# Kernel tuning notes

Measured on AMD Instinct MI355X. Metric: run time of the kernel, lower is better.

## Reference

```python
import jax, jax.numpy as jnp
import numpy as np

HALF_LOG_2PI = 0.5 * float(np.log(2.0 * np.pi))


def setup_inputs() -> dict:
    key = jax.random.key(0)
    k1, k2 = jax.random.split(key)
    N, D = 16384, 2048
    x = jax.random.normal(k1, (N, D), dtype=jnp.float32)
    raw_params = jax.random.normal(k2, (2 * D,), dtype=jnp.float32)
    # chain spanning tree: edges (i, i+1) for i in 0..D-2  -> shape [D-1, 2]
    idx = jnp.arange(D - 1, dtype=jnp.int64)
    edges = jnp.stack([idx, idx + 1], axis=1)
    return {"x": x, "raw_params": raw_params, "edges": edges}


def reference(x, raw_params, edges):
    # x: [N, D] float; raw_params: [2D] float; edges: [E, 2] int
    D = x.shape[1]
    means = jnp.tanh(raw_params[:D]) * 2.0               # [D]
    stds = jax.nn.softplus(raw_params[D:]) + 1e-6         # [D]
    # Each edge (i, j) contributes logN(x_i) + logN(x_j); equivalently each
    # feature k contributes deg(k) * logN(x_k), deg = endpoint multiplicity.
    deg = jnp.zeros((D,), dtype=x.dtype).at[edges.reshape(-1)].add(1.0)  # [D]
    z = (x - means) / stds                                # [N, D]
    logp = -0.5 * z * z - jnp.log(stds) - HALF_LOG_2PI    # [N, D]
    return logp @ deg                                     # [N]
```

## Files before the change

kernel.cpp:

```cpp
#include <hip/hip_runtime.h>
#include <math.h>

#define HALF_LOG_2PI_F 0.9189385332046727f

typedef float f32x4 __attribute__((ext_vector_type(4)));

template <int NI>
__global__ __launch_bounds__(256) void clt_fused(
        const float* __restrict__ x,
        const float* __restrict__ rp,
        const int* __restrict__ edges,
        float* __restrict__ out,
        int D, int E, int N, int total_waves) {
    extern __shared__ __align__(16) float smem[];
    float* sdeg = smem;
    float* As   = smem + D;
    float* Bs   = smem + 2 * D;

    const int tid = threadIdx.x;

    for (int k = tid; k < D; k += 256) sdeg[k] = 0.0f;
    __syncthreads();
    for (int e = tid; e < E; e += 256) {
        atomicAdd(&sdeg[edges[2 * e]], 1.0f);
        atomicAdd(&sdeg[edges[2 * e + 1]], 1.0f);
    }
    __syncthreads();

    float local_c = 0.0f;
    for (int k = tid; k < D; k += 256) {
        float m = tanhf(rp[k]) * 2.0f;
        float sx = rp[D + k];
        float s = fmaxf(sx, 0.0f) + log1pf(expf(-fabsf(sx))) + 1e-6f;
        float inv_s2 = 1.0f / (s * s);
        float deg = sdeg[k];
        As[k] = deg * (-0.5f * inv_s2);
        Bs[k] = deg * (m * inv_s2);
        local_c += deg * (-0.5f * m * m * inv_s2 - logf(s) - HALF_LOG_2PI_F);
    }
#pragma unroll
    for (int off = 32; off > 0; off >>= 1)
        local_c += __shfl_down(local_c, off, 64);
    __shared__ float wsum[4];
    if ((tid & 63) == 0) wsum[tid >> 6] = local_c;
    __syncthreads();
    const float c = wsum[0] + wsum[1] + wsum[2] + wsum[3];

    const int lane = tid & 63;
    const f32x4* Av = (const f32x4*)As;
    const f32x4* Bv = (const f32x4*)Bs;
    f32x4 a4[NI], b4[NI];
#pragma unroll
    for (int i = 0; i < NI; ++i) {
        a4[i] = Av[i * 64 + lane];
        b4[i] = Bv[i * 64 + lane];
    }

    const int gwave = blockIdx.x * 4 + (tid >> 6);
    for (int r = gwave * 2; r < N; r += total_waves * 2) {
        const f32x4* xv0 = (const f32x4*)(x + (size_t)r * (size_t)D);
        const f32x4* xv1 = (const f32x4*)(x + (size_t)(r + 1) * (size_t)D);
        float p0 = 0.0f, q0 = 0.0f, p1 = 0.0f, q1 = 0.0f;
#pragma unroll
        for (int i = 0; i < NI; ++i) {
            f32x4 x0 = __builtin_nontemporal_load(&xv0[i * 64 + lane]);
            f32x4 x1 = __builtin_nontemporal_load(&xv1[i * 64 + lane]);
            p0 += x0.x * fmaf(a4[i].x, x0.x, b4[i].x);
            q0 += x0.y * fmaf(a4[i].y, x0.y, b4[i].y);
            p0 += x0.z * fmaf(a4[i].z, x0.z, b4[i].z);
            q0 += x0.w * fmaf(a4[i].w, x0.w, b4[i].w);
            p1 += x1.x * fmaf(a4[i].x, x1.x, b4[i].x);
            q1 += x1.y * fmaf(a4[i].y, x1.y, b4[i].y);
            p1 += x1.z * fmaf(a4[i].z, x1.z, b4[i].z);
            q1 += x1.w * fmaf(a4[i].w, x1.w, b4[i].w);
        }
        float acc0 = p0 + q0;
        float acc1 = p1 + q1;
#pragma unroll
        for (int off = 32; off > 0; off >>= 1) {
            acc0 += __shfl_down(acc0, off, 64);
            acc1 += __shfl_down(acc1, off, 64);
        }
        if (lane == 0) {
            out[r] = acc0 + c;
            out[r + 1] = acc1 + c;
        }
    }
}

__global__ void clt_prep_kernel(const float* __restrict__ rp,
                                const int* __restrict__ edges,
                                float* __restrict__ A,
                                float* __restrict__ B,
                                float* __restrict__ csum,
                                int D, int E) {
    extern __shared__ float sdeg[];
    for (int k = threadIdx.x; k < D; k += blockDim.x) sdeg[k] = 0.0f;
    __syncthreads();
    for (int e = threadIdx.x; e < E; e += blockDim.x) {
        atomicAdd(&sdeg[edges[2 * e]], 1.0f);
        atomicAdd(&sdeg[edges[2 * e + 1]], 1.0f);
    }
    __syncthreads();
    float local_c = 0.0f;
    for (int k = threadIdx.x; k < D; k += blockDim.x) {
        float m = tanhf(rp[k]) * 2.0f;
        float sx = rp[D + k];
        float s = fmaxf(sx, 0.0f) + log1pf(expf(-fabsf(sx))) + 1e-6f;
        float inv_s2 = 1.0f / (s * s);
        float deg = sdeg[k];
        A[k] = deg * (-0.5f * inv_s2);
        B[k] = deg * (m * inv_s2);
        local_c += deg * (-0.5f * m * m * inv_s2 - logf(s) - HALF_LOG_2PI_F);
    }
    __shared__ float wsum[16];
    for (int off = 32; off > 0; off >>= 1)
        local_c += __shfl_down(local_c, off, 64);
    if ((threadIdx.x & 63) == 0) wsum[threadIdx.x >> 6] = local_c;
    __syncthreads();
    if (threadIdx.x == 0) {
        float t = 0.0f;
        int nw = (blockDim.x + 63) >> 6;
        for (int w = 0; w < nw; ++w) t += wsum[w];
        *csum = t;
    }
}

__global__ __launch_bounds__(256) void clt_row_generic(
        const float* __restrict__ x,
        const float* __restrict__ A,
        const float* __restrict__ B,
        const float* __restrict__ csum,
        float* __restrict__ out,
        int D) {
    const int row = blockIdx.x;
    float acc = 0.0f;
    for (int k = threadIdx.x; k < D; k += blockDim.x) {
        float xs = x[(size_t)row * (size_t)D + k];
        acc += xs * fmaf(A[k], xs, B[k]);
    }
    for (int off = 32; off > 0; off >>= 1)
        acc += __shfl_down(acc, off, 64);
    __shared__ float wsum[4];
    if ((threadIdx.x & 63) == 0) wsum[threadIdx.x >> 6] = acc;
    __syncthreads();
    if (threadIdx.x == 0)
        out[row] = wsum[0] + wsum[1] + wsum[2] + wsum[3] + *csum;
}

extern "C" void kernel_launch(void* const* d_in, const int* in_sizes, int n_in,
                              void* d_out, int out_size, void* d_ws, size_t ws_size,
                              hipStream_t stream) {
    const float* x     = (const float*)d_in[0];
    const float* rp    = (const float*)d_in[1];
    const int*   edges = (const int*)d_in[2];
    float* out = (float*)d_out;

    const int D = in_sizes[1] / 2;
    const int E = in_sizes[2] / 2;
    const int N = out_size;

    const int NI = D / 256;
    const bool fast = (D % 256 == 0) && (N % 2 == 0) &&
                      (NI == 2 || NI == 4 || NI == 8 || NI == 16);
    if (fast) {
        const int blocks = 512;
        const int total_waves = blocks * 4;
        const size_t lds = (size_t)3 * D * sizeof(float);
        switch (NI) {
            case 2:  clt_fused<2><<<blocks, 256, lds, stream>>>(x, rp, edges, out, D, E, N, total_waves); break;
            case 4:  clt_fused<4><<<blocks, 256, lds, stream>>>(x, rp, edges, out, D, E, N, total_waves); break;
            case 8:  clt_fused<8><<<blocks, 256, lds, stream>>>(x, rp, edges, out, D, E, N, total_waves); break;
            default: clt_fused<16><<<blocks, 256, lds, stream>>>(x, rp, edges, out, D, E, N, total_waves); break;
        }
    } else {
        float* A    = (float*)d_ws;
        float* B    = A + D;
        float* csum = B + D;
        clt_prep_kernel<<<1, 1024, D * sizeof(float), stream>>>(rp, edges, A, B, csum, D, E);
        clt_row_generic<<<N, 256, 0, stream>>>(x, A, B, csum, out, D);
    }
}
```

Measured before the change: 39.44 us.

## Split parameter prep into separate kernel and drop per-block redundant prep

Replaces the fused kernel, in which every block recomputed the degree histogram and the A/B coefficients, with one single-block prep kernel that writes A, B and the constant to workspace. A streaming row kernel then reads those coefficients from global memory. The change also doubles the grid to 1024 blocks with a min-blocks launch bound, and switches the x loads from nontemporal to ordinary loads. It removes the per-block prep work and the LDS use, at the cost of an extra kernel launch and a serial dependency on one small single-block kernel.

Result: slower. 75.00 us (+90.1%).

```diff
diff --git a/kernel.cpp b/kernel.cpp
--- a/kernel.cpp
+++ b/kernel.cpp
@@ -4,89 +4,6 @@
 #define HALF_LOG_2PI_F 0.9189385332046727f
 
 typedef float f32x4 __attribute__((ext_vector_type(4)));
-
-template <int NI>
-__global__ __launch_bounds__(256) void clt_fused(
-        const float* __restrict__ x,
-        const float* __restrict__ rp,
-        const int* __restrict__ edges,
-        float* __restrict__ out,
-        int D, int E, int N, int total_waves) {
-    extern __shared__ __align__(16) float smem[];
-    float* sdeg = smem;
-    float* As   = smem + D;
-    float* Bs   = smem + 2 * D;
-
-    const int tid = threadIdx.x;
-
-    for (int k = tid; k < D; k += 256) sdeg[k] = 0.0f;
-    __syncthreads();
-    for (int e = tid; e < E; e += 256) {
-        atomicAdd(&sdeg[edges[2 * e]], 1.0f);
-        atomicAdd(&sdeg[edges[2 * e + 1]], 1.0f);
-    }
-    __syncthreads();
-
-    float local_c = 0.0f;
-    for (int k = tid; k < D; k += 256) {
-        float m = tanhf(rp[k]) * 2.0f;
-        float sx = rp[D + k];
-        float s = fmaxf(sx, 0.0f) + log1pf(expf(-fabsf(sx))) + 1e-6f;
-        float inv_s2 = 1.0f / (s * s);
-        float deg = sdeg[k];
-        As[k] = deg * (-0.5f * inv_s2);
-        Bs[k] = deg * (m * inv_s2);
-        local_c += deg * (-0.5f * m * m * inv_s2 - logf(s) - HALF_LOG_2PI_F);
-    }
-#pragma unroll
-    for (int off = 32; off > 0; off >>= 1)
-        local_c += __shfl_down(local_c, off, 64);
-    __shared__ float wsum[4];
-    if ((tid & 63) == 0) wsum[tid >> 6] = local_c;
-    __syncthreads();
-    const float c = wsum[0] + wsum[1] + wsum[2] + wsum[3];
-
-    const int lane = tid & 63;
-    const f32x4* Av = (const f32x4*)As;
-    const f32x4* Bv = (const f32x4*)Bs;
-    f32x4 a4[NI], b4[NI];
-#pragma unroll
-    for (int i = 0; i < NI; ++i) {
-        a4[i] = Av[i * 64 + lane];
-        b4[i] = Bv[i * 64 + lane];
-    }
-
-    const int gwave = blockIdx.x * 4 + (tid >> 6);
-    for (int r = gwave * 2; r < N; r += total_waves * 2) {
-        const f32x4* xv0 = (const f32x4*)(x + (size_t)r * (size_t)D);
-        const f32x4* xv1 = (const f32x4*)(x + (size_t)(r + 1) * (size_t)D);
-        float p0 = 0.0f, q0 = 0.0f, p1 = 0.0f, q1 = 0.0f;
-#pragma unroll
-        for (int i = 0; i < NI; ++i) {
-            f32x4 x0 = __builtin_nontemporal_load(&xv0[i * 64 + lane]);
-            f32x4 x1 = __builtin_nontemporal_load(&xv1[i * 64 + lane]);
-            p0 += x0.x * fmaf(a4[i].x, x0.x, b4[i].x);
-            q0 += x0.y * fmaf(a4[i].y, x0.y, b4[i].y);
-            p0 += x0.z * fmaf(a4[i].z, x0.z, b4[i].z);
-            q0 += x0.w * fmaf(a4[i].w, x0.w, b4[i].w);
-            p1 += x1.x * fmaf(a4[i].x, x1.x, b4[i].x);
-            q1 += x1.y * fmaf(a4[i].y, x1.y, b4[i].y);
-            p1 += x1.z * fmaf(a4[i].z, x1.z, b4[i].z);
-            q1 += x1.w * fmaf(a4[i].w, x1.w, b4[i].w);
-        }
-        float acc0 = p0 + q0;
-        float acc1 = p1 + q1;
-#pragma unroll
-        for (int off = 32; off > 0; off >>= 1) {
-            acc0 += __shfl_down(acc0, off, 64);
-            acc1 += __shfl_down(acc1, off, 64);
-        }
-        if (lane == 0) {
-            out[r] = acc0 + c;
-            out[r + 1] = acc1 + c;
-        }
-    }
-}
 
 __global__ void clt_prep_kernel(const float* __restrict__ rp,
                                 const int* __restrict__ edges,
@@ -126,6 +43,58 @@
     }
 }
 
+template <int NI>
+__global__ __launch_bounds__(256, 4) void clt_rows2(
+        const float* __restrict__ x,
+        const float* __restrict__ A,
+        const float* __restrict__ B,
+        const float* __restrict__ csum,
+        float* __restrict__ out,
+        int D, int N, int total_waves) {
+    const int lane = threadIdx.x & 63;
+    const int gwave = blockIdx.x * 4 + (threadIdx.x >> 6);
+
+    const f32x4* Av = (const f32x4*)A;
+    const f32x4* Bv = (const f32x4*)B;
+    f32x4 a4[NI], b4[NI];
+#pragma unroll
+    for (int i = 0; i < NI; ++i) {
+        a4[i] = Av[i * 64 + lane];
+        b4[i] = Bv[i * 64 + lane];
+    }
+    const float c = *csum;
+
+    for (int r = gwave * 2; r < N; r += total_waves * 2) {
+        const f32x4* xv0 = (const f32x4*)(x + (size_t)r * (size_t)D);
+        const f32x4* xv1 = (const f32x4*)(x + (size_t)(r + 1) * (size_t)D);
+        float p0 = 0.0f, q0 = 0.0f, p1 = 0.0f, q1 = 0.0f;
+#pragma unroll
+        for (int i = 0; i < NI; ++i) {
+            f32x4 x0 = xv0[i * 64 + lane];
+            f32x4 x1 = xv1[i * 64 + lane];
+            p0 += x0.x * fmaf(a4[i].x, x0.x, b4[i].x);
+            q0 += x0.y * fmaf(a4[i].y, x0.y, b4[i].y);
+            p0 += x0.z * fmaf(a4[i].z, x0.z, b4[i].z);
+            q0 += x0.w * fmaf(a4[i].w, x0.w, b4[i].w);
+            p1 += x1.x * fmaf(a4[i].x, x1.x, b4[i].x);
+            q1 += x1.y * fmaf(a4[i].y, x1.y, b4[i].y);
+            p1 += x1.z * fmaf(a4[i].z, x1.z, b4[i].z);
+            q1 += x1.w * fmaf(a4[i].w, x1.w, b4[i].w);
+        }
+        float acc0 = p0 + q0;
+        float acc1 = p1 + q1;
+#pragma unroll
+        for (int off = 32; off > 0; off >>= 1) {
+            acc0 += __shfl_down(acc0, off, 64);
+            acc1 += __shfl_down(acc1, off, 64);
+        }
+        if (lane == 0) {
+            out[r] = acc0 + c;
+            out[r + 1] = acc1 + c;
+        }
+    }
+}
+
 __global__ __launch_bounds__(256) void clt_row_generic(
         const float* __restrict__ x,
         const float* __restrict__ A,
@@ -160,24 +129,24 @@
     const int E = in_sizes[2] / 2;
     const int N = out_size;
 
+    float* A    = (float*)d_ws;
+    float* B    = A + D;
+    float* csum = B + D;
+
+    clt_prep_kernel<<<1, 1024, D * sizeof(float), stream>>>(rp, edges, A, B, csum, D, E);
+
     const int NI = D / 256;
-    const bool fast = (D % 256 == 0) && (N % 2 == 0) &&
-                      (NI == 2 || NI == 4 || NI == 8 || NI == 16);
-    if (fast) {
-        const int blocks = 512;
+    if (D % 256 == 0 && N % 2 == 0 &&
+        (NI == 2 || NI == 4 || NI == 8 || NI == 16)) {
+        const int blocks = 1024;
         const int total_waves = blocks * 4;
-        const size_t lds = (size_t)3 * D * sizeof(float);
         switch (NI) {
-            case 2:  clt_fused<2><<<blocks, 256, lds, stream>>>(x, rp, edges, out, D, E, N, total_waves); break;
-            case 4:  clt_fused<4><<<blocks, 256, lds, stream>>>(x, rp, edges, out, D, E, N, total_waves); break;
-            case 8:  clt_fused<8><<<blocks, 256, lds, stream>>>(x, rp, edges, out, D, E, N, total_waves); break;
-            default: clt_fused<16><<<blocks, 256, lds, stream>>>(x, rp, edges, out, D, E, N, total_waves); break;
+            case 2:  clt_rows2<2><<<blocks, 256, 0, stream>>>(x, A, B, csum, out, D, N, total_waves); break;
+            case 4:  clt_rows2<4><<<blocks, 256, 0, stream>>>(x, A, B, csum, out, D, N, total_waves); break;
+            case 8:  clt_rows2<8><<<blocks, 256, 0, stream>>>(x, A, B, csum, out, D, N, total_waves); break;
+            default: clt_rows2<16><<<blocks, 256, 0, stream>>>(x, A, B, csum, out, D, N, total_waves); break;
         }
     } else {
-        float* A    = (float*)d_ws;
-        float* B    = A + D;
-        float* csum = B + D;
-        clt_prep_kernel<<<1, 1024, D * sizeof(float), stream>>>(rp, edges, A, B, csum, D, E);
         clt_row_generic<<<N, 256, 0, stream>>>(x, A, B, csum, out, D);
     }
 }
```
